# Kernel tuning notes

Measured on AMD Instinct MI355X. Metric: run time of the kernel, lower is better.

Reference implementation:

```python
import jax, jax.numpy as jnp
import numpy as np
import math

LOCAL_RADIUS = 2
NEG_INF = -1e9


def _bilinear_gather_shared(feat, sample):
    """Bilinear sample with zeros padding, align_corners=True semantics.
    feat: [b, c, h, w]; sample: [n, k, 2] pixel coords (x, y), shared across batch.
    Returns [b, c, n, k].
    """
    b, c, h, w = feat.shape
    x, y = sample[..., 0], sample[..., 1]  # [n, k]
    x0 = jnp.floor(x); y0 = jnp.floor(y)
    x1 = x0 + 1.0;     y1 = y0 + 1.0
    feat_flat = feat.reshape(b, c, h * w)

    def corner(xi, yi, wgt):
        valid = (xi >= 0) & (xi < w) & (yi >= 0) & (yi < h)
        xi_c = jnp.clip(xi, 0, w - 1).astype(jnp.int32)
        yi_c = jnp.clip(yi, 0, h - 1).astype(jnp.int32)
        idx = yi_c * w + xi_c                       # [n, k]
        vals = feat_flat[:, :, idx]                 # [b, c, n, k]
        wv = jnp.where(valid, wgt, 0.0)             # zeros padding
        return vals * wv[None, None]

    out = (corner(x0, y0, (x1 - x) * (y1 - y))
           + corner(x1, y0, (x - x0) * (y1 - y))
           + corner(x0, y1, (x1 - x) * (y - y0))
           + corner(x1, y1, (x - x0) * (y - y0)))
    return out


def local_correlation_softmax(f0, f1, radius):
    b, c, h, w = f0.shape
    ygrid, xgrid = jnp.meshgrid(jnp.arange(h, dtype=f0.dtype),
                                jnp.arange(w, dtype=f0.dtype), indexing='ij')
    coords = jnp.stack([xgrid, ygrid], axis=-1).reshape(h * w, 2)  # [n, 2] (x, y)

    offs = jnp.arange(-radius, radius + 1, dtype=f0.dtype)
    dyy, dxx = jnp.meshgrid(offs, offs, indexing='ij')
    win = jnp.stack([dxx, dyy], axis=-1).reshape(-1, 2)            # [K, 2]

    sample = coords[:, None, :] + win[None, :, :]                  # [n, K, 2]
    valid = ((sample[..., 0] >= 0) & (sample[..., 0] < w)
             & (sample[..., 1] >= 0) & (sample[..., 1] < h))       # [n, K]

    win_feat = _bilinear_gather_shared(f1, sample)                 # [b, c, n, K]
    f0_flat = f0.reshape(b, c, h * w)
    corr = jnp.einsum('bcn,bcnk->bnk', f0_flat, win_feat) / (c ** 0.5)
    corr = jnp.where(valid[None], corr, NEG_INF)
    prob = jax.nn.softmax(corr, axis=-1)                           # [b, n, K]
    corresp = jnp.einsum('bnk,nkt->bnt', prob, sample)             # [b, n, 2]
    corresp = corresp.reshape(b, h, w, 2).transpose(0, 3, 1, 2)    # [b, 2, h, w]
    init = jnp.stack([xgrid, ygrid], axis=0)[None]                 # [1, 2, h, w]
    return corresp - init


def setup_inputs() -> dict:
    key = jax.random.key(0)
    k0, k1, k2 = jax.random.split(key, 3)
    shape = (2, 64, 128, 128)
    return {
        'feature0': jax.random.normal(k0, shape, dtype=jnp.float32),
        'feature1': jax.random.normal(k1, shape, dtype=jnp.float32),
        'feature2': jax.random.normal(k2, shape, dtype=jnp.float32),
    }


def reference(feature0, feature1, feature2):
    r = LOCAL_RADIUS
    v_0_2 = local_correlation_softmax(feature0, feature2, r)
    v_1_2 = local_correlation_softmax(feature1, feature2, r)
    v_2_0 = local_correlation_softmax(feature2, feature0, r)
    v_2_1 = local_correlation_softmax(feature2, feature1, r)
    return jnp.stack([v_0_2, v_1_2, v_2_0, v_2_1], axis=0)  # [4, b, 2, h, w]
```

## Files before the change

kernel.cpp:

```cpp
#include <hip/hip_runtime.h>

#define H 128
#define W 128
#define C 64
#define HW (H * W)
#define RAD 2
#define KD 5
#define KK 25

#define TSX 16
#define TSY 8
#define HROWS 12
#define RSTR 24
#define PSTR 292
#define NPAIR 32
#define LDSU (NPAIR * PSTR)

typedef _Float16 h2 __attribute__((ext_vector_type(2)));

__device__ __forceinline__ float dot2acc(h2 a, h2 w, float acc)
{
#if __has_builtin(__builtin_amdgcn_fdot2)
    return __builtin_amdgcn_fdot2(a, w, acc, false);
#else
    return fmaf((float)a.x, (float)w.x, fmaf((float)a.y, (float)w.y, acc));
#endif
}

__device__ __forceinline__ uint32_t pkh2(float lo, float hi)
{
    h2 t; t.x = (_Float16)lo; t.y = (_Float16)hi;
    return __builtin_bit_cast(uint32_t, t);
}

__device__ __forceinline__ h2 bch2(uint32_t u) { return __builtin_bit_cast(h2, u); }

__device__ __forceinline__ float cs_reduce(float x)
{
    float a = x, b = x;
    asm("v_permlane16_swap_b32 %0, %1" : "+v"(a), "+v"(b));
    float s = a + b;
    float c = s, d = s;
    asm("v_permlane32_swap_b32 %0, %1" : "+v"(c), "+v"(d));
    return c + d;
}

__device__ __forceinline__ float2 softmax_eo(float (&cr)[KK], int xx, int yy)
{
    const float scale = 0.125f;
    float m = -1e30f;
#pragma unroll
    for (int ky = 0; ky < KD; ++ky) {
        int syy = yy + ky - RAD;
#pragma unroll
        for (int kx = 0; kx < KD; ++kx) {
            int sxx = xx + kx - RAD;
            int k = ky * KD + kx;
            float cv = cr[k] * scale;
            bool valid = (sxx >= 0) && (sxx < W) && (syy >= 0) && (syy < H);
            cv = valid ? cv : -1e9f;
            cr[k] = cv;
            m = fmaxf(m, cv);
        }
    }
    float sum = 0.f, ox = 0.f, oy = 0.f;
#pragma unroll
    for (int ky = 0; ky < KD; ++ky)
#pragma unroll
        for (int kx = 0; kx < KD; ++kx) {
            int k = ky * KD + kx;
            float e = __expf(cr[k] - m);
            sum += e;
            ox += e * (float)(kx - RAD);
            oy += e * (float)(ky - RAD);
        }
    float inv = 1.f / sum;
    return make_float2(ox * inv, oy * inv);
}

__global__ __launch_bounds__(256, 4)
void bam_corr_softmax_kernel(const float* __restrict__ f0,
                             const float* __restrict__ f1,
                             const float* __restrict__ f2,
                             float* __restrict__ out)
{
    __shared__ uint32_t lds[LDSU];

    const int tid  = threadIdx.x;
    const int lane = tid & 63;
    const int wav  = tid >> 6;
    const int cs   = lane >> 4;
    const int s    = lane & 15;
    const int sy   = s >> 2;
    const int sxp  = s & 3;
    const int wx   = wav & 1;
    const int wy   = wav >> 1;
    const int lx   = wx * 8 + sxp * 2;
    const int ly   = wy * 4 + sy;

    const int i     = blockIdx.x;
    const int band  = i & 7;
    const int j     = i >> 3;
    const int img   = j & 7;
    const int t     = j >> 3;
    const int tileX = t & 7;
    const int tileY = band * 2 + (t >> 3);

    const int v = img >> 1;
    const int b = img & 1;

    const float* A;
    const float* Bf;
    if (v == 0)      { A = f0; Bf = f2; }
    else if (v == 1) { A = f1; Bf = f2; }
    else if (v == 2) { A = f2; Bf = f0; }
    else             { A = f2; Bf = f1; }

    const int x0 = tileX * TSX;
    const int y0 = tileY * TSY;
    const int x  = x0 + lx;
    const int y  = y0 + ly;

    const float* Arow  = A + (size_t)b * C * HW + (size_t)(y * W + x);
    const float* Bbase = Bf + (size_t)b * C * HW;

    const bool interior = (tileX >= 1) && (tileX <= 6) && (tileY >= 1) && (tileY <= 14);
#pragma unroll
    for (int it = 0; it < 9; ++it) {
        int q   = tid + it * 256;
        int p   = q / 72;
        int rem = q - p * 72;
        int row = rem / 6;
        int c6  = rem - row * 6;
        int gy  = y0 - 2 + row;
        int gx  = x0 - 4 + c6 * 4;
        float4 lo, hi;
        if (interior) {
            const float* p0 = Bbase + (size_t)(2 * p) * HW + (size_t)(gy * W + gx);
            lo = *reinterpret_cast<const float4*>(p0);
            hi = *reinterpret_cast<const float4*>(p0 + HW);
        } else {
            float lv[4], hv[4];
#pragma unroll
            for (int e = 0; e < 4; ++e) {
                int gxe = gx + e;
                bool ok = (gy >= 0) && (gy < H) && (gxe >= 0) && (gxe < W);
                size_t off = (size_t)(2 * p) * HW + (size_t)(ok ? gy * W + gxe : 0);
                lv[e] = ok ? Bbase[off] : 0.f;
                hv[e] = ok ? Bbase[off + HW] : 0.f;
            }
            lo = make_float4(lv[0], lv[1], lv[2], lv[3]);
            hi = make_float4(hv[0], hv[1], hv[2], hv[3]);
        }
        uint4 wq = make_uint4(pkh2(lo.x, hi.x), pkh2(lo.y, hi.y),
                              pkh2(lo.z, hi.z), pkh2(lo.w, hi.w));
        *reinterpret_cast<uint4*>(&lds[p * PSTR + row * RSTR + c6 * 4]) = wq;
    }
    __syncthreads();

    float c0[KK], c1[KK];
#pragma unroll
    for (int k = 0; k < KK; ++k) { c0[k] = 0.f; c1[k] = 0.f; }

#pragma unroll
    for (int c = 0; c < 8; ++c) {
        const int pl = cs * 8 + c;
        const float* ap = Arow + (size_t)(2 * pl) * HW;
        float2 alo = *reinterpret_cast<const float2*>(ap);
        float2 ahi = *reinterpret_cast<const float2*>(ap + HW);
        h2 a0, a1;
        a0.x = (_Float16)alo.x; a0.y = (_Float16)ahi.x;
        a1.x = (_Float16)alo.y; a1.y = (_Float16)ahi.y;
        const uint32_t* bp = &lds[pl * PSTR + ly * RSTR + lx + 2];
#pragma unroll
        for (int rr = 0; rr < KD; ++rr) {
            const uint32_t* rp = bp + rr * RSTR;
            uint2 u01 = *reinterpret_cast<const uint2*>(rp);
            uint2 u23 = *reinterpret_cast<const uint2*>(rp + 2);
            uint2 u45 = *reinterpret_cast<const uint2*>(rp + 4);
            h2 w0 = bch2(u01.x), w1 = bch2(u01.y), w2 = bch2(u23.x);
            h2 w3 = bch2(u23.y), w4 = bch2(u45.x), w5 = bch2(u45.y);
            const int kb = rr * KD;
            c0[kb + 0] = dot2acc(a0, w0, c0[kb + 0]);
            c0[kb + 1] = dot2acc(a0, w1, c0[kb + 1]);
            c0[kb + 2] = dot2acc(a0, w2, c0[kb + 2]);
            c0[kb + 3] = dot2acc(a0, w3, c0[kb + 3]);
            c0[kb + 4] = dot2acc(a0, w4, c0[kb + 4]);
            c1[kb + 0] = dot2acc(a1, w1, c1[kb + 0]);
            c1[kb + 1] = dot2acc(a1, w2, c1[kb + 1]);
            c1[kb + 2] = dot2acc(a1, w3, c1[kb + 2]);
            c1[kb + 3] = dot2acc(a1, w4, c1[kb + 3]);
            c1[kb + 4] = dot2acc(a1, w5, c1[kb + 4]);
        }
    }

#pragma unroll
    for (int k = 0; k < KK; ++k) {
        c0[k] = cs_reduce(c0[k]);
        c1[k] = cs_reduce(c1[k]);
    }

    float2 r0 = softmax_eo(c0, x,     y);
    float2 r1 = softmax_eo(c1, x + 1, y);

    if (cs == 0) {
        size_t ob = ((size_t)img * 2) * HW + (size_t)(y * W + x);
        *reinterpret_cast<float2*>(&out[ob])      = make_float2(r0.x, r1.x);
        *reinterpret_cast<float2*>(&out[ob + HW]) = make_float2(r0.y, r1.y);
    }
}

extern "C" void kernel_launch(void* const* d_in, const int* in_sizes, int n_in,
                              void* d_out, int out_size, void* d_ws, size_t ws_size,
                              hipStream_t stream)
{
    const float* f0 = (const float*)d_in[0];
    const float* f1 = (const float*)d_in[1];
    const float* f2 = (const float*)d_in[2];
    float* out = (float*)d_out;

    dim3 block(256, 1, 1);
    dim3 grid(1024, 1, 1);
    bam_corr_softmax_kernel<<<grid, block, 0, stream>>>(f0, f1, f2, out);
}
```

Measured before the change: 26.19 us.

## Halve tile width, split channels 8-way with two-phase LDS staging

Shrinks the spatial tile to 8x8 and doubles the grid. The channel reduction is split across 8 lanes, reduced with xor shuffles in place of permlane swaps, and the B halo is staged through LDS in two channel halves separated by barriers. LDS per block drops, so occupancy can rise (launch bounds now 7 blocks). The softmax skips masking on interior tiles and uses exp2 with a prescaled log2e factor. In exchange the halo is re-read more often relative to tile area, and an extra barrier is added per block.

```diff
diff --git a/kernel.cpp b/kernel.cpp
--- a/kernel.cpp
+++ b/kernel.cpp
@@ -8,13 +8,15 @@
 #define KD 5
 #define KK 25
 
-#define TSX 16
+#define TSX 8
 #define TSY 8
 #define HROWS 12
 #define RSTR 24
-#define PSTR 292
-#define NPAIR 32
-#define LDSU (NPAIR * PSTR)
+#define PSTR 288
+#define GSTR 580
+#define LDSU (8 * GSTR)
+
+#define SCALE_L2E 0.18033688011112042f
 
 typedef _Float16 h2 __attribute__((ext_vector_type(2)));
 
@@ -32,33 +34,31 @@
     h2 t; t.x = (_Float16)lo; t.y = (_Float16)hi;
     return __builtin_bit_cast(uint32_t, t);
 }
-
 __device__ __forceinline__ h2 bch2(uint32_t u) { return __builtin_bit_cast(h2, u); }
 
 __device__ __forceinline__ float cs_reduce(float x)
 {
-    float a = x, b = x;
-    asm("v_permlane16_swap_b32 %0, %1" : "+v"(a), "+v"(b));
-    float s = a + b;
-    float c = s, d = s;
-    asm("v_permlane32_swap_b32 %0, %1" : "+v"(c), "+v"(d));
-    return c + d;
-}
-
+    x += __shfl_xor(x, 1, 64);
+    x += __shfl_xor(x, 2, 64);
+    x += __shfl_xor(x, 4, 64);
+    return x;
+}
+
+template<bool MASKED>
 __device__ __forceinline__ float2 softmax_eo(float (&cr)[KK], int xx, int yy)
 {
-    const float scale = 0.125f;
     float m = -1e30f;
 #pragma unroll
     for (int ky = 0; ky < KD; ++ky) {
-        int syy = yy + ky - RAD;
 #pragma unroll
         for (int kx = 0; kx < KD; ++kx) {
-            int sxx = xx + kx - RAD;
             int k = ky * KD + kx;
-            float cv = cr[k] * scale;
-            bool valid = (sxx >= 0) && (sxx < W) && (syy >= 0) && (syy < H);
-            cv = valid ? cv : -1e9f;
+            float cv = cr[k] * SCALE_L2E;
+            if (MASKED) {
+                int sxx = xx + kx - RAD, syy = yy + ky - RAD;
+                bool valid = (sxx >= 0) && (sxx < W) && (syy >= 0) && (syy < H);
+                cv = valid ? cv : -1e9f;
+            }
             cr[k] = cv;
             m = fmaxf(m, cv);
         }
@@ -69,7 +69,7 @@
 #pragma unroll
         for (int kx = 0; kx < KD; ++kx) {
             int k = ky * KD + kx;
-            float e = __expf(cr[k] - m);
+            float e = exp2f(cr[k] - m);
             sum += e;
             ox += e * (float)(kx - RAD);
             oy += e * (float)(ky - RAD);
@@ -78,7 +78,7 @@
     return make_float2(ox * inv, oy * inv);
 }
 
-__global__ __launch_bounds__(256, 4)
+__global__ __launch_bounds__(256, 7)
 void bam_corr_softmax_kernel(const float* __restrict__ f0,
                              const float* __restrict__ f1,
                              const float* __restrict__ f2,
@@ -89,22 +89,20 @@
     const int tid  = threadIdx.x;
     const int lane = tid & 63;
     const int wav  = tid >> 6;
-    const int cs   = lane >> 4;
-    const int s    = lane & 15;
-    const int sy   = s >> 2;
-    const int sxp  = s & 3;
-    const int wx   = wav & 1;
-    const int wy   = wav >> 1;
-    const int lx   = wx * 8 + sxp * 2;
-    const int ly   = wy * 4 + sy;
+    const int cs   = lane & 7;
+    const int slot = lane >> 3;
+    const int sx2  = slot & 3;
+    const int syw  = slot >> 2;
+    const int lx   = sx2 * 2;
+    const int ly   = wav * 2 + syw;
 
     const int i     = blockIdx.x;
     const int band  = i & 7;
     const int j     = i >> 3;
     const int img   = j & 7;
     const int t     = j >> 3;
-    const int tileX = t & 7;
-    const int tileY = band * 2 + (t >> 3);
+    const int tileX = t & 15;
+    const int tileY = band * 2 + (t >> 4);
 
     const int v = img >> 1;
     const int b = img & 1;
@@ -124,73 +122,88 @@
     const float* Arow  = A + (size_t)b * C * HW + (size_t)(y * W + x);
     const float* Bbase = Bf + (size_t)b * C * HW;
 
-    const bool interior = (tileX >= 1) && (tileX <= 6) && (tileY >= 1) && (tileY <= 14);
-#pragma unroll
-    for (int it = 0; it < 9; ++it) {
-        int q   = tid + it * 256;
-        int p   = q / 72;
-        int rem = q - p * 72;
-        int row = rem / 6;
-        int c6  = rem - row * 6;
-        int gy  = y0 - 2 + row;
-        int gx  = x0 - 4 + c6 * 4;
-        float4 lo, hi;
-        if (interior) {
-            const float* p0 = Bbase + (size_t)(2 * p) * HW + (size_t)(gy * W + gx);
-            lo = *reinterpret_cast<const float4*>(p0);
-            hi = *reinterpret_cast<const float4*>(p0 + HW);
-        } else {
-            float lv[4], hv[4];
-#pragma unroll
-            for (int e = 0; e < 4; ++e) {
-                int gxe = gx + e;
-                bool ok = (gy >= 0) && (gy < H) && (gxe >= 0) && (gxe < W);
-                size_t off = (size_t)(2 * p) * HW + (size_t)(ok ? gy * W + gxe : 0);
-                lv[e] = ok ? Bbase[off] : 0.f;
-                hv[e] = ok ? Bbase[off + HW] : 0.f;
-            }
-            lo = make_float4(lv[0], lv[1], lv[2], lv[3]);
-            hi = make_float4(hv[0], hv[1], hv[2], hv[3]);
-        }
-        uint4 wq = make_uint4(pkh2(lo.x, hi.x), pkh2(lo.y, hi.y),
-                              pkh2(lo.z, hi.z), pkh2(lo.w, hi.w));
-        *reinterpret_cast<uint4*>(&lds[p * PSTR + row * RSTR + c6 * 4]) = wq;
-    }
-    __syncthreads();
-
-    float c0[KK], c1[KK];
-#pragma unroll
-    for (int k = 0; k < KK; ++k) { c0[k] = 0.f; c1[k] = 0.f; }
-
-#pragma unroll
-    for (int c = 0; c < 8; ++c) {
-        const int pl = cs * 8 + c;
-        const float* ap = Arow + (size_t)(2 * pl) * HW;
+    const bool interior = (tileX >= 1) && (tileX <= 14) && (tileY >= 1) && (tileY <= 14);
+
+    uint32_t a0c[4], a1c[4];
+#pragma unroll
+    for (int q = 0; q < 4; ++q) {
+        int r = q >> 1, c = q & 1;
+        int pair = r * 16 + cs * 2 + c;
+        const float* ap = Arow + (size_t)(2 * pair) * HW;
         float2 alo = *reinterpret_cast<const float2*>(ap);
         float2 ahi = *reinterpret_cast<const float2*>(ap + HW);
-        h2 a0, a1;
-        a0.x = (_Float16)alo.x; a0.y = (_Float16)ahi.x;
-        a1.x = (_Float16)alo.y; a1.y = (_Float16)ahi.y;
-        const uint32_t* bp = &lds[pl * PSTR + ly * RSTR + lx + 2];
-#pragma unroll
-        for (int rr = 0; rr < KD; ++rr) {
-            const uint32_t* rp = bp + rr * RSTR;
-            uint2 u01 = *reinterpret_cast<const uint2*>(rp);
-            uint2 u23 = *reinterpret_cast<const uint2*>(rp + 2);
-            uint2 u45 = *reinterpret_cast<const uint2*>(rp + 4);
-            h2 w0 = bch2(u01.x), w1 = bch2(u01.y), w2 = bch2(u23.x);
-            h2 w3 = bch2(u23.y), w4 = bch2(u45.x), w5 = bch2(u45.y);
-            const int kb = rr * KD;
-            c0[kb + 0] = dot2acc(a0, w0, c0[kb + 0]);
-            c0[kb + 1] = dot2acc(a0, w1, c0[kb + 1]);
-            c0[kb + 2] = dot2acc(a0, w2, c0[kb + 2]);
-            c0[kb + 3] = dot2acc(a0, w3, c0[kb + 3]);
-            c0[kb + 4] = dot2acc(a0, w4, c0[kb + 4]);
-            c1[kb + 0] = dot2acc(a1, w1, c1[kb + 0]);
-            c1[kb + 1] = dot2acc(a1, w2, c1[kb + 1]);
-            c1[kb + 2] = dot2acc(a1, w3, c1[kb + 2]);
-            c1[kb + 3] = dot2acc(a1, w4, c1[kb + 3]);
-            c1[kb + 4] = dot2acc(a1, w5, c1[kb + 4]);
+        a0c[q] = pkh2(alo.x, ahi.x);
+        a1c[q] = pkh2(alo.y, ahi.y);
+    }
+
+    float c0[KK], c1[KK];
+#pragma unroll
+    for (int k = 0; k < KK; ++k) { c0[k] = 0.f; c1[k] = 0.f; }
+
+#pragma unroll
+    for (int r = 0; r < 2; ++r) {
+        if (r) __syncthreads();
+
+#pragma unroll
+        for (int it = 0; it < 3; ++it) {
+            int q   = tid + it * 256;
+            int p   = q / 48;
+            int rem = q - p * 48;
+            int row = rem >> 2;
+            int c4  = rem & 3;
+            int gy  = y0 - 2 + row;
+            int gx  = x0 - 4 + c4 * 4;
+            int ch0 = 2 * (r * 16 + p);
+            float4 lo, hi;
+            if (interior) {
+                const float* p0 = Bbase + (size_t)ch0 * HW + (size_t)(gy * W + gx);
+                lo = *reinterpret_cast<const float4*>(p0);
+                hi = *reinterpret_cast<const float4*>(p0 + HW);
+            } else {
+                float lv[4], hv[4];
+#pragma unroll
+                for (int e = 0; e < 4; ++e) {
+                    int gxe = gx + e;
+                    bool ok = (gy >= 0) && (gy < H) && (gxe >= 0) && (gxe < W);
+                    size_t off = (size_t)ch0 * HW + (size_t)(ok ? gy * W + gxe : 0);
+                    lv[e] = ok ? Bbase[off] : 0.f;
+                    hv[e] = ok ? Bbase[off + HW] : 0.f;
+                }
+                lo = make_float4(lv[0], lv[1], lv[2], lv[3]);
+                hi = make_float4(hv[0], hv[1], hv[2], hv[3]);
+            }
+            uint4 wq = make_uint4(pkh2(lo.x, hi.x), pkh2(lo.y, hi.y),
+                                  pkh2(lo.z, hi.z), pkh2(lo.w, hi.w));
+            int g = p >> 1, c = p & 1;
+            *reinterpret_cast<uint4*>(&lds[g * GSTR + c * PSTR + row * RSTR + c4 * 4]) = wq;
+        }
+        __syncthreads();
+
+#pragma unroll
+        for (int c = 0; c < 2; ++c) {
+            h2 a0 = bch2(a0c[r * 2 + c]);
+            h2 a1 = bch2(a1c[r * 2 + c]);
+            const uint32_t* bp = &lds[cs * GSTR + c * PSTR + ly * RSTR + lx + 2];
+#pragma unroll
+            for (int rr = 0; rr < KD; ++rr) {
+                const uint32_t* rp = bp + rr * RSTR;
+                uint2 u01 = *reinterpret_cast<const uint2*>(rp);
+                uint2 u23 = *reinterpret_cast<const uint2*>(rp + 2);
+                uint2 u45 = *reinterpret_cast<const uint2*>(rp + 4);
+                h2 w0 = bch2(u01.x), w1 = bch2(u01.y), w2 = bch2(u23.x);
+                h2 w3 = bch2(u23.y), w4 = bch2(u45.x), w5 = bch2(u45.y);
+                const int kb = rr * KD;
+                c0[kb + 0] = dot2acc(a0, w0, c0[kb + 0]);
+                c0[kb + 1] = dot2acc(a0, w1, c0[kb + 1]);
+                c0[kb + 2] = dot2acc(a0, w2, c0[kb + 2]);
+                c0[kb + 3] = dot2acc(a0, w3, c0[kb + 3]);
+                c0[kb + 4] = dot2acc(a0, w4, c0[kb + 4]);
+                c1[kb + 0] = dot2acc(a1, w1, c1[kb + 0]);
+                c1[kb + 1] = dot2acc(a1, w2, c1[kb + 1]);
+                c1[kb + 2] = dot2acc(a1, w3, c1[kb + 2]);
+                c1[kb + 3] = dot2acc(a1, w4, c1[kb + 3]);
+                c1[kb + 4] = dot2acc(a1, w5, c1[kb + 4]);
+            }
         }
     }
 
@@ -200,8 +213,14 @@
         c1[k] = cs_reduce(c1[k]);
     }
 
-    float2 r0 = softmax_eo(c0, x,     y);
-    float2 r1 = softmax_eo(c1, x + 1, y);
+    float2 r0, r1;
+    if (interior) {
+        r0 = softmax_eo<false>(c0, x,     y);
+        r1 = softmax_eo<false>(c1, x + 1, y);
+    } else {
+        r0 = softmax_eo<true>(c0, x,     y);
+        r1 = softmax_eo<true>(c1, x + 1, y);
+    }
 
     if (cs == 0) {
         size_t ob = ((size_t)img * 2) * HW + (size_t)(y * W + x);
@@ -220,6 +239,6 @@
     float* out = (float*)d_out;
 
     dim3 block(256, 1, 1);
-    dim3 grid(1024, 1, 1);
+    dim3 grid(2048, 1, 1);
     bam_corr_softmax_kernel<<<grid, block, 0, stream>>>(f0, f1, f2, out);
 }
```

New measurement: 82.74 us. 3.16x slower.

## Hoist A-feature loads before LDS fill and simplify softmax without max subtraction

Applied to the files above, without the earlier changes.

Loads and packs the query features into registers before staging the window tile into LDS, so their global loads overlap with the tile fill. The softmax drops the max-subtraction pass, folds the scale into an exp2 multiplier, and applies boundary masking only for edge tiles through a template. The channel-split reduction switches from permlane swap instructions to shfl_xor, and fp16 packing uses cvt_pkrtz. Skipping the max subtraction relies on correlation magnitudes staying small enough for exp not to overflow. Holding the query features in registers for the whole fill adds register pressure.

```diff
diff --git a/kernel.cpp b/kernel.cpp
--- a/kernel.cpp
+++ b/kernel.cpp
@@ -16,7 +16,10 @@
 #define NPAIR 32
 #define LDSU (NPAIR * PSTR)
 
+#define SCALE_L2E 0.18033688011112042f
+
 typedef _Float16 h2 __attribute__((ext_vector_type(2)));
+typedef __fp16 fp16v2 __attribute__((ext_vector_type(2)));
 
 __device__ __forceinline__ float dot2acc(h2 a, h2 w, float acc)
 {
@@ -29,51 +32,44 @@
 
 __device__ __forceinline__ uint32_t pkh2(float lo, float hi)
 {
+#if __has_builtin(__builtin_amdgcn_cvt_pkrtz)
+    fp16v2 t = __builtin_amdgcn_cvt_pkrtz(lo, hi);
+    return __builtin_bit_cast(uint32_t, t);
+#else
     h2 t; t.x = (_Float16)lo; t.y = (_Float16)hi;
     return __builtin_bit_cast(uint32_t, t);
+#endif
 }
 
 __device__ __forceinline__ h2 bch2(uint32_t u) { return __builtin_bit_cast(h2, u); }
 
 __device__ __forceinline__ float cs_reduce(float x)
 {
-    float a = x, b = x;
-    asm("v_permlane16_swap_b32 %0, %1" : "+v"(a), "+v"(b));
-    float s = a + b;
-    float c = s, d = s;
-    asm("v_permlane32_swap_b32 %0, %1" : "+v"(c), "+v"(d));
-    return c + d;
-}
-
-__device__ __forceinline__ float2 softmax_eo(float (&cr)[KK], int xx, int yy)
-{
-    const float scale = 0.125f;
-    float m = -1e30f;
+    x += __shfl_xor(x, 16, 64);
+    x += __shfl_xor(x, 32, 64);
+    return x;
+}
+
+template<bool MASKED>
+__device__ __forceinline__ float2 softmax_eo(const float (&cr)[KK], int xx, int yy)
+{
+    float sum = 0.f, ox = 0.f, oy = 0.f;
 #pragma unroll
     for (int ky = 0; ky < KD; ++ky) {
-        int syy = yy + ky - RAD;
-#pragma unroll
-        for (int kx = 0; kx < KD; ++kx) {
-            int sxx = xx + kx - RAD;
-            int k = ky * KD + kx;
-            float cv = cr[k] * scale;
-            bool valid = (sxx >= 0) && (sxx < W) && (syy >= 0) && (syy < H);
-            cv = valid ? cv : -1e9f;
-            cr[k] = cv;
-            m = fmaxf(m, cv);
-        }
-    }
-    float sum = 0.f, ox = 0.f, oy = 0.f;
-#pragma unroll
-    for (int ky = 0; ky < KD; ++ky)
 #pragma unroll
         for (int kx = 0; kx < KD; ++kx) {
             int k = ky * KD + kx;
-            float e = __expf(cr[k] - m);
+            float e = exp2f(cr[k] * SCALE_L2E);
+            if (MASKED) {
+                int sxx = xx + kx - RAD, syy = yy + ky - RAD;
+                bool valid = (sxx >= 0) && (sxx < W) && (syy >= 0) && (syy < H);
+                e = valid ? e : 0.f;
+            }
             sum += e;
             ox += e * (float)(kx - RAD);
             oy += e * (float)(ky - RAD);
         }
+    }
     float inv = 1.f / sum;
     return make_float2(ox * inv, oy * inv);
 }
@@ -125,6 +121,18 @@
     const float* Bbase = Bf + (size_t)b * C * HW;
 
     const bool interior = (tileX >= 1) && (tileX <= 6) && (tileY >= 1) && (tileY <= 14);
+
+    uint32_t a0c[8], a1c[8];
+#pragma unroll
+    for (int c = 0; c < 8; ++c) {
+        const int pl = cs * 8 + c;
+        const float* ap = Arow + (size_t)(2 * pl) * HW;
+        float2 alo = *reinterpret_cast<const float2*>(ap);
+        float2 ahi = *reinterpret_cast<const float2*>(ap + HW);
+        a0c[c] = pkh2(alo.x, ahi.x);
+        a1c[c] = pkh2(alo.y, ahi.y);
+    }
+
 #pragma unroll
     for (int it = 0; it < 9; ++it) {
         int q   = tid + it * 256;
@@ -165,12 +173,8 @@
 #pragma unroll
     for (int c = 0; c < 8; ++c) {
         const int pl = cs * 8 + c;
-        const float* ap = Arow + (size_t)(2 * pl) * HW;
-        float2 alo = *reinterpret_cast<const float2*>(ap);
-        float2 ahi = *reinterpret_cast<const float2*>(ap + HW);
-        h2 a0, a1;
-        a0.x = (_Float16)alo.x; a0.y = (_Float16)ahi.x;
-        a1.x = (_Float16)alo.y; a1.y = (_Float16)ahi.y;
+        h2 a0 = bch2(a0c[c]);
+        h2 a1 = bch2(a1c[c]);
         const uint32_t* bp = &lds[pl * PSTR + ly * RSTR + lx + 2];
 #pragma unroll
         for (int rr = 0; rr < KD; ++rr) {
@@ -200,8 +204,14 @@
         c1[k] = cs_reduce(c1[k]);
     }
 
-    float2 r0 = softmax_eo(c0, x,     y);
-    float2 r1 = softmax_eo(c1, x + 1, y);
+    float2 r0, r1;
+    if (interior) {
+        r0 = softmax_eo<false>(c0, x,     y);
+        r1 = softmax_eo<false>(c1, x + 1, y);
+    } else {
+        r0 = softmax_eo<true>(c0, x,     y);
+        r1 = softmax_eo<true>(c1, x + 1, y);
+    }
 
     if (cs == 0) {
         size_t ob = ((size_t)img * 2) * HW + (size_t)(y * W + x);
```

Measured after the change: 27.96 us. 1.07x slower.
